# Performance work log

Measured on AMD Instinct MI355X. Metric: run time of the kernel, lower is better.

## Reference

```python
import jax, jax.numpy as jnp
import numpy as np

MAX_DISPLACEMENT = 4  # matches init_kwargs
EPS = 1e-12  # torch F.normalize clamp


def _l2_normalize(x):
    # L2 normalize over channel dim (axis=1), matching torch.nn.functional.normalize
    n = jnp.sqrt(jnp.sum(x * x, axis=1, keepdims=True))
    return x / jnp.maximum(n, EPS)


def setup_inputs() -> dict:
    key = jax.random.key(0)
    k1, k2 = jax.random.split(key)
    B, C, H, W = 16, 256, 64, 64
    fA = jax.random.normal(k1, (B, C, H, W), dtype=jnp.float32)
    fB = jax.random.normal(k2, (B, C, H, W), dtype=jnp.float32)
    return {"fA": fA, "fB": fB}


def reference(fA, fB):
    d = MAX_DISPLACEMENT
    B, C, H, W = fA.shape
    fAn = _l2_normalize(fA)
    fBn = _l2_normalize(fB)
    # zero-pad fB by d (matches F.unfold padding=d), then take shifted windows.
    fBp = jnp.pad(fBn, ((0, 0), (0, 0), (d, d), (d, d)))
    outs = []
    # Fixed structural loop over (2d+1)^2 = 81 displacements (row-major ky, kx,
    # matching F.unfold's kernel-position ordering). No huge patch tensor is
    # materialized; each term is a channel dot-product of fA with shifted fB.
    for dy in range(2 * d + 1):
        for dx in range(2 * d + 1):
            shifted = jax.lax.dynamic_slice(
                fBp, (0, 0, dy, dx), (B, C, H, W))
            outs.append(jnp.sum(fAn * shifted, axis=1))  # (B, H, W)
    return jnp.stack(outs, axis=1)  # (B, (2d+1)^2, H, W)
```

## Files before the change

kernel.cpp:

```cpp
#include <hip/hip_runtime.h>
#include <hip/hip_bf16.h>
#include <math.h>

typedef short short8 __attribute__((ext_vector_type(8)));
typedef float f32x16 __attribute__((ext_vector_type(16)));

#define BB 16
#define CC 256
#define HH 64
#define WW 64
#define HWX 4096
#define DD 4
#define KD 9
#define KK 81
#define NSLOT 10

#define RAW_BAR() do { \
    asm volatile("s_waitcnt lgkmcnt(0)" ::: "memory"); \
    __builtin_amdgcn_s_barrier(); \
} while (0)

__device__ __forceinline__ short bf16c(float x) {
    __hip_bfloat16 h = __float2bfloat16(x);
    return *reinterpret_cast<short*>(&h);
}

__device__ __forceinline__ int lds_byte(int w, int c) {
    return (w * 512 + c * 2) ^ ((w & 31) << 4);
}

__device__ __forceinline__ void b_issue16(const float* __restrict__ row,
                                          int c0, int l, float* v) {
    #pragma unroll
    for (int j = 0; j < 16; ++j)
        v[j] = row[(size_t)(c0 + j) * HWX + l];
}

__device__ __forceinline__ float b_commit16(const float* v, unsigned short* bufp,
                                            int c0, int l) {
    float ss = 0.f;
    #pragma unroll
    for (int j = 0; j < 16; ++j) ss += v[j] * v[j];
    #pragma unroll
    for (int h = 0; h < 2; ++h) {
        short8 st;
        #pragma unroll
        for (int j = 0; j < 8; ++j) st[j] = bf16c(v[h * 8 + j]);
        *(short8*)((char*)bufp + lds_byte(l, c0 + h * 8)) = st;
    }
    return ss;
}

__global__ __launch_bounds__(512) void corr_mfma(
    const float* __restrict__ fA, const float* __restrict__ fB,
    float* __restrict__ out)
{
    __shared__ __attribute__((aligned(16))) unsigned short buf[2][WW * CC];
    __shared__ float part[2][8 * WW];
    __shared__ float invA_ls[2][WW];

    const int bid = blockIdx.x;
    const int swzb = (bid & 7) * 64 + (bid >> 3);
    const int b = swzb >> 5, jr = swzb & 31;
    const int h0 = 2 * jr;

    const int tid = threadIdx.x;
    const int l = tid & 63;
    const int wvu = __builtin_amdgcn_readfirstlane(tid >> 6);
    const int g = wvu >> 2;
    const int q = wvu & 3;
    const int hg = h0 + g;
    const int ti = q >> 1, tj = q & 1;
    const int ml = l & 31, kg = l >> 5;
    const int m = ti * 32 + ml;
    const int n = tj * 32 + ml;

    const float* Abase = fA + (size_t)b * CC * HWX + hg * WW;
    {
        float ss = 0.f;
        #pragma unroll
        for (int r = 0; r < 8; ++r) {
            const int c = q * 64 + r * 8;
            float v[8]; short8 st;
            #pragma unroll
            for (int j = 0; j < 8; ++j) v[j] = Abase[(size_t)(c + j) * HWX + l];
            #pragma unroll
            for (int j = 0; j < 8; ++j) ss += v[j] * v[j];
            #pragma unroll
            for (int j = 0; j < 8; ++j) st[j] = bf16c(v[j]);
            *(short8*)((char*)buf[g] + lds_byte(l, c)) = st;
        }
        part[1][wvu * 64 + l] = ss;
    }
    __syncthreads();
    if (tid < 2 * WW) {
        const int gg = tid >> 6, ll = tid & 63;
        float s = part[1][(gg * 4 + 0) * 64 + ll] + part[1][(gg * 4 + 1) * 64 + ll]
                + part[1][(gg * 4 + 2) * 64 + ll] + part[1][(gg * 4 + 3) * 64 + ll];
        invA_ls[gg][ll] = 1.f / fmaxf(sqrtf(s), 1e-12f);
    }
    short8 afr[16];
    #pragma unroll
    for (int s = 0; s < 16; ++s)
        afr[s] = *(const short8*)((const char*)buf[g] + lds_byte(m, s * 16 + kg * 8));
    __syncthreads();
    {
        const float iam = invA_ls[g][m];
        #pragma unroll
        for (int s = 0; s < 16; ++s) {
            short8 t = afr[s];
            #pragma unroll
            for (int j = 0; j < 8; ++j) {
                union { unsigned u; float f; } uu;
                uu.u = ((unsigned)(unsigned short)t[j]) << 16;
                t[j] = bf16c(uu.f * iam);
            }
            afr[s] = t;
        }
    }
    const float* fBb = fB + (size_t)b * CC * HWX;
    {
        const int hb0 = h0 - DD;
        if ((unsigned)hb0 < HH) {
            const float* row = fBb + (size_t)hb0 * WW;
            float v[16];
            b_issue16(row, wvu * 32, l, v);
            float ss = b_commit16(v, buf[0], wvu * 32, l);
            b_issue16(row, wvu * 32 + 16, l, v);
            ss += b_commit16(v, buf[0], wvu * 32 + 16, l);
            part[0][wvu * 64 + l] = ss;
        }
    }
    __syncthreads();

    for (int r = 0; r < NSLOT; ++r) {
        const int cur = r & 1;
        const int hb = h0 - DD + r;
        const bool vcur = (unsigned)hb < HH;
        const bool vnext = (r + 1 < NSLOT) && ((unsigned)(hb + 1) < HH);
        const int dy = r - g;
        const bool dyv = (dy >= 0 && dy < KD);
        const bool comp = dyv && vcur;
        const float* nrow = fBb + (size_t)(hb + 1) * WW;
        float* ob = out + (((size_t)b * KK + dy * KD) * HH + hg) * WW;

        float v[16];
        if (vnext) b_issue16(nrow, wvu * 32, l, v);

        f32x16 acc;
        if (comp) {
            #pragma unroll
            for (int i = 0; i < 16; ++i) acc[i] = 0.f;
            __builtin_amdgcn_s_setprio(1);
            #pragma unroll
            for (int s = 0; s < 8; ++s) {
                short8 bfr = *(const short8*)((const char*)buf[cur] + lds_byte(n, s * 16 + kg * 8));
                acc = __builtin_amdgcn_mfma_f32_32x32x16_bf16(afr[s], bfr, acc, 0, 0, 0);
            }
            __builtin_amdgcn_s_setprio(0);
        }

        float ssn = 0.f;
        if (vnext) {
            ssn = b_commit16(v, buf[cur ^ 1], wvu * 32, l);
            b_issue16(nrow, wvu * 32 + 16, l, v);
        }

        if (comp) {
            __builtin_amdgcn_s_setprio(1);
            #pragma unroll
            for (int s = 8; s < 16; ++s) {
                short8 bfr = *(const short8*)((const char*)buf[cur] + lds_byte(n, s * 16 + kg * 8));
                acc = __builtin_amdgcn_mfma_f32_32x32x16_bf16(afr[s], bfr, acc, 0, 0, 0);
            }
            __builtin_amdgcn_s_setprio(0);
            float sB = 0.f;
            #pragma unroll
            for (int qq = 0; qq < 8; ++qq) sB += part[cur][qq * 64 + n];
            const float ibn = 1.f / fmaxf(sqrtf(sB), 1e-12f);
            #pragma unroll
            for (int rr = 0; rr < 16; ++rr) {
                const int w = ti * 32 + (rr & 3) + 8 * (rr >> 2) + 4 * kg;
                const int dx = n - w + 4;
                if (dx >= 0 && dx < KD)
                    ob[(size_t)dx * HWX + w] = acc[rr] * ibn;
            }
            if (q == 3) {
                int i = -1;
                if (l < 10) i = l;
                else if (l >= 16 && l < 26) i = l - 16;
                if (i >= 0) {
                    const int wz0 = (i < 4) ? 0 : (i < 7) ? 1 : (i < 9) ? 2 : 3;
                    const int dx0 = i - ((wz0 == 0) ? 0 : (wz0 == 1) ? 4 : (wz0 == 2) ? 7 : 9);
                    const int wz = (l < 10) ? wz0 : 63 - wz0;
                    const int dxz = (l < 10) ? dx0 : 8 - dx0;
                    ob[(size_t)dxz * HWX + wz] = 0.f;
                }
            }
        } else if (dyv) {
            for (int i = q * 64 + l; i < KD * WW; i += 256)
                ob[(size_t)(i >> 6) * HWX + (i & 63)] = 0.f;
        }

        if (vnext) {
            ssn += b_commit16(v, buf[cur ^ 1], wvu * 32 + 16, l);
            part[cur ^ 1][wvu * 64 + l] = ssn;
        }
        RAW_BAR();
    }
}

extern "C" void kernel_launch(void* const* d_in, const int* in_sizes, int n_in,
                              void* d_out, int out_size, void* d_ws, size_t ws_size,
                              hipStream_t stream) {
    const float* fA = (const float*)d_in[0];
    const float* fB = (const float*)d_in[1];
    float* outp = (float*)d_out;
    corr_mfma<<<dim3(BB * HH / 2), 512, 0, stream>>>(fA, fB, outp);
}
```

Baseline: 60.06 us.

## Process four output rows per block to reuse each fB row across more outputs

```diff
diff --git a/kernel.cpp b/kernel.cpp
--- a/kernel.cpp
+++ b/kernel.cpp
@@ -13,7 +13,8 @@
 #define DD 4
 #define KD 9
 #define KK 81
-#define NSLOT 10
+#define GR 4
+#define NSLOT 12
 
 #define RAW_BAR() do { \
     asm volatile("s_waitcnt lgkmcnt(0)" ::: "memory"); \
@@ -57,67 +58,77 @@
 {
     __shared__ __attribute__((aligned(16))) unsigned short buf[2][WW * CC];
     __shared__ float part[2][8 * WW];
-    __shared__ float invA_ls[2][WW];
+    __shared__ float invA_ls[GR][WW];
 
     const int bid = blockIdx.x;
-    const int swzb = (bid & 7) * 64 + (bid >> 3);
-    const int b = swzb >> 5, jr = swzb & 31;
-    const int h0 = 2 * jr;
+    const int swzb = (bid & 7) * 32 + (bid >> 3);
+    const int b = swzb >> 4, jr = swzb & 15;
+    const int h0 = 4 * jr;
 
     const int tid = threadIdx.x;
     const int l = tid & 63;
     const int wvu = __builtin_amdgcn_readfirstlane(tid >> 6);
-    const int g = wvu >> 2;
-    const int q = wvu & 3;
+    const int g = wvu >> 1;
+    const int tj = wvu & 1;
     const int hg = h0 + g;
-    const int ti = q >> 1, tj = q & 1;
     const int ml = l & 31, kg = l >> 5;
-    const int m = ti * 32 + ml;
     const int n = tj * 32 + ml;
 
-    const float* Abase = fA + (size_t)b * CC * HWX + hg * WW;
-    {
-        float ss = 0.f;
-        #pragma unroll
-        for (int r = 0; r < 8; ++r) {
-            const int c = q * 64 + r * 8;
-            float v[8]; short8 st;
-            #pragma unroll
-            for (int j = 0; j < 8; ++j) v[j] = Abase[(size_t)(c + j) * HWX + l];
-            #pragma unroll
-            for (int j = 0; j < 8; ++j) ss += v[j] * v[j];
-            #pragma unroll
-            for (int j = 0; j < 8; ++j) st[j] = bf16c(v[j]);
-            *(short8*)((char*)buf[g] + lds_byte(l, c)) = st;
-        }
-        part[1][wvu * 64 + l] = ss;
-    }
-    __syncthreads();
-    if (tid < 2 * WW) {
-        const int gg = tid >> 6, ll = tid & 63;
-        float s = part[1][(gg * 4 + 0) * 64 + ll] + part[1][(gg * 4 + 1) * 64 + ll]
-                + part[1][(gg * 4 + 2) * 64 + ll] + part[1][(gg * 4 + 3) * 64 + ll];
-        invA_ls[gg][ll] = 1.f / fmaxf(sqrtf(s), 1e-12f);
-    }
-    short8 afr[16];
-    #pragma unroll
-    for (int s = 0; s < 16; ++s)
-        afr[s] = *(const short8*)((const char*)buf[g] + lds_byte(m, s * 16 + kg * 8));
-    __syncthreads();
-    {
-        const float iam = invA_ls[g][m];
-        #pragma unroll
-        for (int s = 0; s < 16; ++s) {
-            short8 t = afr[s];
-            #pragma unroll
-            for (int j = 0; j < 8; ++j) {
-                union { unsigned u; float f; } uu;
-                uu.u = ((unsigned)(unsigned short)t[j]) << 16;
-                t[j] = bf16c(uu.f * iam);
-            }
-            afr[s] = t;
-        }
-    }
+    short8 afrL[16], afrH[16];
+    #pragma unroll
+    for (int t = 0; t < 2; ++t) {
+        {
+            const int rs = wvu >> 2;
+            const int cq = wvu & 3;
+            const float* Ar = fA + (size_t)b * CC * HWX + (h0 + 2 * t + rs) * WW;
+            float ss = 0.f;
+            #pragma unroll
+            for (int r = 0; r < 8; ++r) {
+                const int c = cq * 64 + r * 8;
+                float v[8]; short8 st;
+                #pragma unroll
+                for (int j = 0; j < 8; ++j) v[j] = Ar[(size_t)(c + j) * HWX + l];
+                #pragma unroll
+                for (int j = 0; j < 8; ++j) ss += v[j] * v[j];
+                #pragma unroll
+                for (int j = 0; j < 8; ++j) st[j] = bf16c(v[j]);
+                *(short8*)((char*)buf[rs] + lds_byte(l, c)) = st;
+            }
+            part[1][wvu * 64 + l] = ss;
+        }
+        __syncthreads();
+        if (tid < 2 * WW) {
+            const int rs = tid >> 6, ll = tid & 63;
+            float s = part[1][(rs * 4 + 0) * 64 + ll] + part[1][(rs * 4 + 1) * 64 + ll]
+                    + part[1][(rs * 4 + 2) * 64 + ll] + part[1][(rs * 4 + 3) * 64 + ll];
+            invA_ls[2 * t + rs][ll] = 1.f / fmaxf(sqrtf(s), 1e-12f);
+        }
+        if ((g >> 1) == t) {
+            #pragma unroll
+            for (int s = 0; s < 16; ++s) {
+                afrL[s] = *(const short8*)((const char*)buf[g & 1] + lds_byte(ml,      s * 16 + kg * 8));
+                afrH[s] = *(const short8*)((const char*)buf[g & 1] + lds_byte(32 + ml, s * 16 + kg * 8));
+            }
+        }
+        __syncthreads();
+        if ((g >> 1) == t) {
+            const float ia0 = invA_ls[g][ml], ia1 = invA_ls[g][32 + ml];
+            #pragma unroll
+            for (int s = 0; s < 16; ++s) {
+                short8 t0 = afrL[s], t1 = afrH[s];
+                #pragma unroll
+                for (int j = 0; j < 8; ++j) {
+                    union { unsigned u; float f; } u0, u1;
+                    u0.u = ((unsigned)(unsigned short)t0[j]) << 16;
+                    u1.u = ((unsigned)(unsigned short)t1[j]) << 16;
+                    t0[j] = bf16c(u0.f * ia0);
+                    t1[j] = bf16c(u1.f * ia1);
+                }
+                afrL[s] = t0; afrH[s] = t1;
+            }
+        }
+    }
+
     const float* fBb = fB + (size_t)b * CC * HWX;
     {
         const int hb0 = h0 - DD;
@@ -147,15 +158,16 @@
         float v[16];
         if (vnext) b_issue16(nrow, wvu * 32, l, v);
 
-        f32x16 acc;
+        f32x16 acc0, acc1;
         if (comp) {
             #pragma unroll
-            for (int i = 0; i < 16; ++i) acc[i] = 0.f;
+            for (int i = 0; i < 16; ++i) { acc0[i] = 0.f; acc1[i] = 0.f; }
             __builtin_amdgcn_s_setprio(1);
             #pragma unroll
             for (int s = 0; s < 8; ++s) {
                 short8 bfr = *(const short8*)((const char*)buf[cur] + lds_byte(n, s * 16 + kg * 8));
-                acc = __builtin_amdgcn_mfma_f32_32x32x16_bf16(afr[s], bfr, acc, 0, 0, 0);
+                acc0 = __builtin_amdgcn_mfma_f32_32x32x16_bf16(afrL[s], bfr, acc0, 0, 0, 0);
+                acc1 = __builtin_amdgcn_mfma_f32_32x32x16_bf16(afrH[s], bfr, acc1, 0, 0, 0);
             }
             __builtin_amdgcn_s_setprio(0);
         }
@@ -171,7 +183,8 @@
             #pragma unroll
             for (int s = 8; s < 16; ++s) {
                 short8 bfr = *(const short8*)((const char*)buf[cur] + lds_byte(n, s * 16 + kg * 8));
-                acc = __builtin_amdgcn_mfma_f32_32x32x16_bf16(afr[s], bfr, acc, 0, 0, 0);
+                acc0 = __builtin_amdgcn_mfma_f32_32x32x16_bf16(afrL[s], bfr, acc0, 0, 0, 0);
+                acc1 = __builtin_amdgcn_mfma_f32_32x32x16_bf16(afrH[s], bfr, acc1, 0, 0, 0);
             }
             __builtin_amdgcn_s_setprio(0);
             float sB = 0.f;
@@ -180,12 +193,15 @@
             const float ibn = 1.f / fmaxf(sqrtf(sB), 1e-12f);
             #pragma unroll
             for (int rr = 0; rr < 16; ++rr) {
-                const int w = ti * 32 + (rr & 3) + 8 * (rr >> 2) + 4 * kg;
-                const int dx = n - w + 4;
-                if (dx >= 0 && dx < KD)
-                    ob[(size_t)dx * HWX + w] = acc[rr] * ibn;
-            }
-            if (q == 3) {
+                const int wf = (rr & 3) + 8 * (rr >> 2) + 4 * kg;
+                const int dx0 = n - wf + 4;
+                if (dx0 >= 0 && dx0 < KD)
+                    ob[(size_t)dx0 * HWX + wf] = acc0[rr] * ibn;
+                const int dx1 = dx0 - 32;
+                if (dx1 >= 0 && dx1 < KD)
+                    ob[(size_t)dx1 * HWX + 32 + wf] = acc1[rr] * ibn;
+            }
+            if (tj == 1) {
                 int i = -1;
                 if (l < 10) i = l;
                 else if (l >= 16 && l < 26) i = l - 16;
@@ -198,7 +214,7 @@
                 }
             }
         } else if (dyv) {
-            for (int i = q * 64 + l; i < KD * WW; i += 256)
+            for (int i = tj * 64 + l; i < KD * WW; i += 128)
                 ob[(size_t)(i >> 6) * HWX + (i & 63)] = 0.f;
         }
 
@@ -216,5 +232,5 @@
     const float* fA = (const float*)d_in[0];
     const float* fB = (const float*)d_in[1];
     float* outp = (float*)d_out;
-    corr_mfma<<<dim3(BB * HH / 2), 512, 0, stream>>>(fA, fB, outp);
-}
+    corr_mfma<<<dim3(BB * HH / GR), 512, 0, stream>>>(fA, fB, outp);
+}
```

After: 117.1 us. +95.0%, slower.

## Single-buffer fB row in LDS and stage fA rows sequentially

Applied to the files above, without the earlier changes.

```diff
diff --git a/kernel.cpp b/kernel.cpp
--- a/kernel.cpp
+++ b/kernel.cpp
@@ -55,7 +55,7 @@
     const float* __restrict__ fA, const float* __restrict__ fB,
     float* __restrict__ out)
 {
-    __shared__ __attribute__((aligned(16))) unsigned short buf[2][WW * CC];
+    __shared__ __attribute__((aligned(16))) unsigned short buf[WW * CC];
     __shared__ float part[2][8 * WW];
     __shared__ float invA_ls[2][WW];
 
@@ -75,49 +75,55 @@
     const int m = ti * 32 + ml;
     const int n = tj * 32 + ml;
 
-    const float* Abase = fA + (size_t)b * CC * HWX + hg * WW;
-    {
-        float ss = 0.f;
-        #pragma unroll
-        for (int r = 0; r < 8; ++r) {
-            const int c = q * 64 + r * 8;
-            float v[8]; short8 st;
-            #pragma unroll
-            for (int j = 0; j < 8; ++j) v[j] = Abase[(size_t)(c + j) * HWX + l];
-            #pragma unroll
-            for (int j = 0; j < 8; ++j) ss += v[j] * v[j];
-            #pragma unroll
-            for (int j = 0; j < 8; ++j) st[j] = bf16c(v[j]);
-            *(short8*)((char*)buf[g] + lds_byte(l, c)) = st;
-        }
-        part[1][wvu * 64 + l] = ss;
-    }
-    __syncthreads();
-    if (tid < 2 * WW) {
-        const int gg = tid >> 6, ll = tid & 63;
-        float s = part[1][(gg * 4 + 0) * 64 + ll] + part[1][(gg * 4 + 1) * 64 + ll]
-                + part[1][(gg * 4 + 2) * 64 + ll] + part[1][(gg * 4 + 3) * 64 + ll];
-        invA_ls[gg][ll] = 1.f / fmaxf(sqrtf(s), 1e-12f);
-    }
     short8 afr[16];
     #pragma unroll
-    for (int s = 0; s < 16; ++s)
-        afr[s] = *(const short8*)((const char*)buf[g] + lds_byte(m, s * 16 + kg * 8));
-    __syncthreads();
-    {
-        const float iam = invA_ls[g][m];
-        #pragma unroll
-        for (int s = 0; s < 16; ++s) {
-            short8 t = afr[s];
-            #pragma unroll
-            for (int j = 0; j < 8; ++j) {
-                union { unsigned u; float f; } uu;
-                uu.u = ((unsigned)(unsigned short)t[j]) << 16;
-                t[j] = bf16c(uu.f * iam);
-            }
-            afr[s] = t;
-        }
-    }
+    for (int t = 0; t < 2; ++t) {
+        {
+            const float* Ar = fA + (size_t)b * CC * HWX + (size_t)(h0 + t) * WW;
+            float ss = 0.f;
+            #pragma unroll
+            for (int r2 = 0; r2 < 4; ++r2) {
+                const int c = wvu * 32 + r2 * 8;
+                float v[8]; short8 st;
+                #pragma unroll
+                for (int j = 0; j < 8; ++j) v[j] = Ar[(size_t)(c + j) * HWX + l];
+                #pragma unroll
+                for (int j = 0; j < 8; ++j) ss += v[j] * v[j];
+                #pragma unroll
+                for (int j = 0; j < 8; ++j) st[j] = bf16c(v[j]);
+                *(short8*)((char*)buf + lds_byte(l, c)) = st;
+            }
+            part[1][wvu * 64 + l] = ss;
+        }
+        __syncthreads();
+        if (tid < WW) {
+            float s = 0.f;
+            #pragma unroll
+            for (int qq = 0; qq < 8; ++qq) s += part[1][qq * 64 + tid];
+            invA_ls[t][tid] = 1.f / fmaxf(sqrtf(s), 1e-12f);
+        }
+        if (g == t) {
+            #pragma unroll
+            for (int s = 0; s < 16; ++s)
+                afr[s] = *(const short8*)((const char*)buf + lds_byte(m, s * 16 + kg * 8));
+        }
+        __syncthreads();
+        if (g == t) {
+            const float iam = invA_ls[t][m];
+            #pragma unroll
+            for (int s = 0; s < 16; ++s) {
+                short8 tt = afr[s];
+                #pragma unroll
+                for (int j = 0; j < 8; ++j) {
+                    union { unsigned u; float f; } uu;
+                    uu.u = ((unsigned)(unsigned short)tt[j]) << 16;
+                    tt[j] = bf16c(uu.f * iam);
+                }
+                afr[s] = tt;
+            }
+        }
+    }
+
     const float* fBb = fB + (size_t)b * CC * HWX;
     {
         const int hb0 = h0 - DD;
@@ -125,16 +131,15 @@
             const float* row = fBb + (size_t)hb0 * WW;
             float v[16];
             b_issue16(row, wvu * 32, l, v);
-            float ss = b_commit16(v, buf[0], wvu * 32, l);
+            float ss = b_commit16(v, buf, wvu * 32, l);
             b_issue16(row, wvu * 32 + 16, l, v);
-            ss += b_commit16(v, buf[0], wvu * 32 + 16, l);
+            ss += b_commit16(v, buf, wvu * 32 + 16, l);
             part[0][wvu * 64 + l] = ss;
         }
     }
     __syncthreads();
 
     for (int r = 0; r < NSLOT; ++r) {
-        const int cur = r & 1;
         const int hb = h0 - DD + r;
         const bool vcur = (unsigned)hb < HH;
         const bool vnext = (r + 1 < NSLOT) && ((unsigned)(hb + 1) < HH);
@@ -144,39 +149,26 @@
         const float* nrow = fBb + (size_t)(hb + 1) * WW;
         float* ob = out + (((size_t)b * KK + dy * KD) * HH + hg) * WW;
 
-        float v[16];
-        if (vnext) b_issue16(nrow, wvu * 32, l, v);
-
-        f32x16 acc;
+        float va[16], vb[16];
+        if (vnext) {
+            b_issue16(nrow, wvu * 32, l, va);
+            b_issue16(nrow, wvu * 32 + 16, l, vb);
+        }
+
         if (comp) {
+            f32x16 acc;
             #pragma unroll
             for (int i = 0; i < 16; ++i) acc[i] = 0.f;
             __builtin_amdgcn_s_setprio(1);
             #pragma unroll
-            for (int s = 0; s < 8; ++s) {
-                short8 bfr = *(const short8*)((const char*)buf[cur] + lds_byte(n, s * 16 + kg * 8));
-                acc = __builtin_amdgcn_mfma_f32_32x32x16_bf16(afr[s], bfr, acc, 0, 0, 0);
-            }
-            __builtin_amdgcn_s_setprio(0);
-        }
-
-        float ssn = 0.f;
-        if (vnext) {
-            ssn = b_commit16(v, buf[cur ^ 1], wvu * 32, l);
-            b_issue16(nrow, wvu * 32 + 16, l, v);
-        }
-
-        if (comp) {
-            __builtin_amdgcn_s_setprio(1);
-            #pragma unroll
-            for (int s = 8; s < 16; ++s) {
-                short8 bfr = *(const short8*)((const char*)buf[cur] + lds_byte(n, s * 16 + kg * 8));
+            for (int s = 0; s < 16; ++s) {
+                short8 bfr = *(const short8*)((const char*)buf + lds_byte(n, s * 16 + kg * 8));
                 acc = __builtin_amdgcn_mfma_f32_32x32x16_bf16(afr[s], bfr, acc, 0, 0, 0);
             }
             __builtin_amdgcn_s_setprio(0);
             float sB = 0.f;
             #pragma unroll
-            for (int qq = 0; qq < 8; ++qq) sB += part[cur][qq * 64 + n];
+            for (int qq = 0; qq < 8; ++qq) sB += part[r & 1][qq * 64 + n];
             const float ibn = 1.f / fmaxf(sqrtf(sB), 1e-12f);
             #pragma unroll
             for (int rr = 0; rr < 16; ++rr) {
@@ -202,9 +194,11 @@
                 ob[(size_t)(i >> 6) * HWX + (i & 63)] = 0.f;
         }
 
+        RAW_BAR();
         if (vnext) {
-            ssn += b_commit16(v, buf[cur ^ 1], wvu * 32 + 16, l);
-            part[cur ^ 1][wvu * 64 + l] = ssn;
+            float ssn = b_commit16(va, buf, wvu * 32, l);
+            ssn += b_commit16(vb, buf, wvu * 32 + 16, l);
+            part[(r + 1) & 1][wvu * 64 + l] = ssn;
         }
         RAW_BAR();
     }
```

Result: slower. 62.28 us (+3.7%).
